# Performance work log

Hardware: AMD Instinct MI355X
Metric: run time of the kernel (lower is better)

Reference implementation:

```python
import jax, jax.numpy as jnp
import numpy as np

E, D, H, K, DIL, T = 8, 768, 3072, 3, 1, 16384


def _conv1d(x, w, b, dilation):
    # x: [1, C_in, L]; w: [C_out, C_in, K]; torch Conv1d with SAME padding
    pad = dilation * (w.shape[-1] - 1) // 2
    y = jax.lax.conv_general_dilated(
        x, w, window_strides=(1,), padding=[(pad, pad)],
        rhs_dilation=(dilation,), dimension_numbers=("NCH", "OIH", "NCH"))
    return y + b[None, :, None]


def setup_inputs() -> dict:
    key = jax.random.key(0)
    k0, k1, k2, k3, k4 = jax.random.split(key, 5)
    inp = jax.random.normal(k0, (T, D), dtype=jnp.float32)
    fwd_expert_count = jnp.full((E,), T // E, dtype=jnp.int32)
    w1 = jax.random.normal(k1, (E, H, D, K), dtype=jnp.float32) * (1.0 / np.sqrt(D * K))
    b1 = jax.random.normal(k2, (E, H), dtype=jnp.float32) * 0.01
    w2 = jax.random.normal(k3, (E, D, H, K), dtype=jnp.float32) * (1.0 / np.sqrt(H * K))
    b2 = jax.random.normal(k4, (E, D), dtype=jnp.float32) * 0.01
    return {"inp": inp, "fwd_expert_count": fwd_expert_count,
            "w1": w1, "b1": b1, "w2": w2, "b2": b2}


def reference(inp, fwd_expert_count, w1, b1, w2, b2):
    # counts define static per-expert segment lengths (constants w.r.t. compute graph)
    counts = np.asarray(jax.device_get(fwd_expert_count))
    x = inp.T[None]  # [1, D, T]
    outs, idx = [], 0
    for i in range(counts.shape[0]):
        n = int(counts[i])
        if n > 0:
            outs.append(_conv1d(x[:, :, idx:idx + n], w1[i], b1[i], DIL))
            idx += n
    h = jax.nn.gelu(jnp.concatenate(outs, axis=2), approximate=False)  # [1, H, T]
    outs, idx = [], 0
    for i in range(counts.shape[0]):
        n = int(counts[i])
        if n > 0:
            outs.append(_conv1d(h[:, :, idx:idx + n], w2[i], b2[i], DIL))
            idx += n
    y = jnp.concatenate(outs, axis=2)[0]  # [D, T]
    return y.T  # [T, D]
```

## Files before the change

kernel.cpp:

```cpp
#include <hip/hip_runtime.h>
#include <hip/hip_bf16.h>
#include <cstdint>

#define E_   8
#define D_   768
#define H_   3072
#define T_   16384
#define SEG  2048
#define PSEG (SEG + 2)

typedef __attribute__((ext_vector_type(8))) __bf16 bf16x8;
typedef __attribute__((ext_vector_type(4))) float f32x4;
typedef __attribute__((ext_vector_type(4))) unsigned int u32x4;

__device__ inline unsigned short f2bf(float f) {
  union { float f; unsigned int u; } v; v.f = f;
  unsigned int u = v.u;
  u += 0x7fffu + ((u >> 16) & 1u);
  return (unsigned short)(u >> 16);
}

__device__ inline float gelu_fast(float x) {
  const float a = -2.302118131f;
  const float b = -0.102944213f;
  float z = x * __builtin_fmaf(b, x * x, a);
  float e = __builtin_amdgcn_exp2f(z);
  return x * __builtin_amdgcn_rcpf(1.0f + e);
}

__device__ inline void gload16(const unsigned short* g, unsigned short* l) {
  __builtin_amdgcn_global_load_lds(
      (const __attribute__((address_space(1))) unsigned int*)g,
      (__attribute__((address_space(3))) unsigned int*)l, 16, 0, 0);
}

__global__ __launch_bounds__(256) void cvt_x_pad_kernel(const float* __restrict__ in,
                                                        unsigned short* __restrict__ out) {
  const int i = blockIdx.x * 256 + threadIdx.x;
  const int elem = i * 8;
  const int row = elem / D_;
  const int col = elem - row * D_;
  const int prow = (row >> 11) * PSEG + 1 + (row & (SEG - 1));
  const float* p = in + (size_t)row * D_ + col;
  u32x4 v;
#pragma unroll
  for (int j = 0; j < 4; ++j)
    v[j] = (unsigned)f2bf(p[2 * j]) | ((unsigned)f2bf(p[2 * j + 1]) << 16);
  *(u32x4*)(out + (size_t)prow * D_ + col) = v;
}

__global__ __launch_bounds__(256) void zero_guards_kernel(unsigned short* __restrict__ buf,
                                                          int C) {
  const int e = blockIdx.x >> 1;
  const size_t row = (size_t)e * PSEG + (blockIdx.x & 1) * (PSEG - 1);
  for (int c = threadIdx.x; c < C; c += 256) buf[row * C + c] = 0;
}

__global__ __launch_bounds__(256) void cvt_w_kernel(const float* __restrict__ in,
                                                    unsigned short* __restrict__ out,
                                                    int C) {
  int r = blockIdx.x;
  const float* src = in + (size_t)r * C * 3;
  unsigned short* dst = out + (size_t)r * C * 3;
  for (int c = threadIdx.x; c < C; c += 256) {
    float v0 = src[c * 3 + 0], v1 = src[c * 3 + 1], v2 = src[c * 3 + 2];
    dst[0 * C + c] = f2bf(v0);
    dst[1 * C + c] = f2bf(v1);
    dst[2 * C + c] = f2bf(v2);
  }
}

template <int CIN, int COUT, bool DO_GELU>
__global__ __launch_bounds__(512, 2) void conv_gemm8_kernel(
    const unsigned short* __restrict__ A,
    const unsigned short* __restrict__ Bt,
    const float* __restrict__ bias,
    void* __restrict__ Out) {
  __shared__ __align__(16) unsigned short lds[65536];

  constexpr int CSTEPS = CIN / 64;
  constexpr int NT = 3 * CSTEPS;
  constexpr int NTN = COUT / 256;

  const int tid  = threadIdx.x;
  const int wid  = tid >> 6, lane = tid & 63;
  const int wm   = wid >> 2, wn = wid & 3;

  const int bid = blockIdx.x;
  const int e   = bid & 7;
  const int rem = bid >> 3;
  const int mc  = rem / (4 * NTN);
  const int r2  = rem - mc * 4 * NTN;
  const int m0  = (mc * 4 + (r2 & 3)) * 256;
  const int n0  = (r2 >> 2) * 256;

  const int rowoff = tid >> 3;
  const int psrc   = ((lane & 7) ^ (lane >> 3)) * 8;
  const int ko     = (lane >> 4) * 16;
  const int ax     = (lane & 7) << 4;

  const size_t abase = ((size_t)e * PSEG + m0) * CIN;

  f32x4 acc[8][4];
#pragma unroll
  for (int n = 0; n < 4; ++n) {
    const float bv = bias[e * COUT + n0 + wn * 64 + n * 16 + (lane & 15)];
#pragma unroll
    for (int m = 0; m < 8; ++m) acc[m][n] = (f32x4){bv, bv, bv, bv};
  }

#define STAGE_A(kt_, part_) do {                                                     \
    const int ktu_ = (kt_);                                                          \
    const int ktc_ = ktu_ < NT ? ktu_ : NT - 1;    \
    const int k3_  = ktc_ / CSTEPS;                                                  \
    const int c0_  = (ktc_ - k3_ * CSTEPS) * 64;                                     \
    const int buf_ = ktu_ & 1;                                                       \
    _Pragma("unroll")                                                                \
    for (int ii_ = 0; ii_ < 2; ++ii_) {                                              \
      gload16(A + abase + (size_t)(ii_ * 128 + (part_) * 64 + rowoff + k3_) * CIN    \
                  + c0_ + psrc,                                                      \
              (unsigned short*)((char*)lds + buf_ * 32768 + ii_ * 16384 +            \
                                (part_) * 8192 + wid * 1024 + lane * 16));           \
    }                                                                                \
  } while (0)

#define STAGE_B(kt_, h_) do {                                                        \
    const int ktu_ = (kt_);                                                          \
    const int ktc_ = ktu_ < NT ? ktu_ : NT - 1;                                      \
    const int k3_  = ktc_ / CSTEPS;                                                  \
    const int c0_  = (ktc_ - k3_ * CSTEPS) * 64;                                     \
    const int buf_ = ktu_ & 1;                                                       \
    _Pragma("unroll")                                                                \
    for (int ii_ = 0; ii_ < 2; ++ii_) {                                              \
      const int brow_ = n0 + (h_) * 128 + ii_ * 64 + rowoff;                         \
      gload16(Bt + ((size_t)(e * COUT + brow_) * 3 + k3_) * CIN + c0_ + psrc,        \
              (unsigned short*)((char*)lds + 65536 + buf_ * 32768 + (h_) * 16384 +  \
                                ii_ * 8192 + wid * 1024 + lane * 16));               \
    }                                                                                \
  } while (0)

#define FULLBAR() do { asm volatile("" ::: "memory");                                \
                       __builtin_amdgcn_s_barrier();                                 \
                       asm volatile("" ::: "memory"); } while (0)
#define VM6() asm volatile("s_waitcnt vmcnt(6)" ::: "memory")
#define VM4() asm volatile("s_waitcnt vmcnt(4)" ::: "memory")
#define VM_NONE()

#define RA(buf_, mq_, s_, raA_, raB_, RB_) do {                                      \
    const char* Ab_ = (const char*)lds + (buf_) * 32768 + wm * 16384;                \
    if (RB_) {                                                                       \
      const char* Bb_ = (const char*)lds + 65536 + (buf_) * 32768 + (wn >> 1) * 16384; \
      _Pragma("unroll")                                                              \
      for (int n_ = 0; n_ < 4; ++n_)                                                 \
        raB_[n_] = *(const bf16x8*)(Bb_ +                                            \
            ((wn & 1) * 64 + n_ * 16 + (lane & 15)) * 128 + (((s_) * 64 + ko) ^ ax)); \
    }                                                                                \
    _Pragma("unroll")                                                                \
    for (int mi_ = 0; mi_ < 4; ++mi_)                                                \
      raA_[mi_] = *(const bf16x8*)(Ab_ +                                             \
          (((mq_) * 4 + mi_) * 16 + (lane & 15)) * 128 + (((s_) * 64 + ko) ^ ax));   \
  } while (0)

#define PHASE(raBuf_, raMq_, raS_, raA_, raB_, RB_, useA_, useB_, mq_, STAGE_STMT, VMW_) \
  do {                                                                               \
    FULLBAR();                                                                       \
    RA(raBuf_, raMq_, raS_, raA_, raB_, RB_);                                        \
    STAGE_STMT;                                                                      \
    __builtin_amdgcn_s_setprio(1);                                                   \
    _Pragma("unroll")                                                                \
    for (int mi_ = 0; mi_ < 4; ++mi_)                                                \
      _Pragma("unroll")                                                              \
      for (int n_ = 0; n_ < 4; ++n_)                                                 \
        acc[(mq_) * 4 + mi_][n_] = __builtin_amdgcn_mfma_f32_16x16x32_bf16(          \
            useA_[mi_], useB_[n_], acc[(mq_) * 4 + mi_][n_], 0, 0, 0);               \
    __builtin_amdgcn_s_setprio(0);                                                   \
    VMW_();                                                                          \
  } while (0)

  STAGE_B(0, 0); STAGE_B(0, 1); STAGE_A(0, 0); STAGE_A(0, 1);
  STAGE_B(1, 0); STAGE_B(1, 1);
  VM6();
  FULLBAR();

  bf16x8 aFA[4], aFB[4], bFA[4], bFB[4];
  RA(0, 0, 0, aFA, bFA, 1);

  int kt0 = 0;
#pragma unroll 1
  for (int it = 0; it < NT / 2; ++it, kt0 += 2) {
    PHASE(0,    0,   1,   aFB, bFB, 1, aFA, bFA, 0, STAGE_A(kt0 + 1, 0), VM6);
    PHASE(0,    1,   0,   aFA, bFA, 0, aFB, bFB, 0, STAGE_A(kt0 + 1, 1), VM_NONE);
    PHASE(0,    1,   1,   aFB, bFB, 0, aFA, bFA, 1, STAGE_B(kt0 + 2, 0), VM4);
    PHASE(1,    0,   0,   aFA, bFA, 1, aFB, bFB, 1, STAGE_B(kt0 + 2, 1), VM_NONE);
    PHASE(1,    0,   1,   aFB, bFB, 1, aFA, bFA, 0, STAGE_A(kt0 + 2, 0), VM6);
    PHASE(1,    1,   0,   aFA, bFA, 0, aFB, bFB, 0, STAGE_A(kt0 + 2, 1), VM_NONE);
    PHASE(1,    1,   1,   aFB, bFB, 0, aFA, bFA, 1, STAGE_B(kt0 + 3, 0), VM4);
    PHASE(0,    0,   0,   aFA, bFA, 1, aFB, bFB, 1, STAGE_B(kt0 + 3, 1), VM_NONE);
  }

  asm volatile("s_waitcnt vmcnt(0)" ::: "memory");

#undef PHASE
#undef RA
#undef STAGE_A
#undef STAGE_B
#undef FULLBAR
#undef VM6
#undef VM4
#undef VM_NONE

#pragma unroll
  for (int m = 0; m < 8; ++m) {
    const int rowb = m0 + wm * 128 + m * 16 + ((lane >> 4) << 2);
#pragma unroll
    for (int n = 0; n < 4; ++n) {
      const int col = n0 + wn * 64 + n * 16 + (lane & 15);
#pragma unroll
      for (int i = 0; i < 4; ++i) {
        if (DO_GELU) {
          const size_t off = ((size_t)e * PSEG + 1 + rowb + i) * COUT + col;
          ((unsigned short*)Out)[off] = f2bf(gelu_fast(acc[m][n][i]));
        } else {
          const size_t off = ((size_t)e * SEG + rowb + i) * COUT + col;
          ((float*)Out)[off] = acc[m][n][i];
        }
      }
    }
  }
}

extern "C" void kernel_launch(void* const* d_in, const int* in_sizes, int n_in,
                              void* d_out, int out_size, void* d_ws, size_t ws_size,
                              hipStream_t stream) {
  const float* inp = (const float*)d_in[0];
  const float* w1 = (const float*)d_in[2];
  const float* b1 = (const float*)d_in[3];
  const float* w2 = (const float*)d_in[4];
  const float* b2 = (const float*)d_in[5];
  float* out = (float*)d_out;
  char* ws = (char*)d_ws;

  const size_t szXp = (size_t)E_ * PSEG * D_ * 2;
  const size_t szHp = (size_t)E_ * PSEG * H_ * 2;
  const size_t szW1 = (size_t)E_ * H_ * 3 * D_ * 2;
  const size_t szW2 = (size_t)E_ * D_ * 3 * H_ * 2;

  unsigned short* Xp  = (unsigned short*)ws;
  unsigned short* Hp  = (unsigned short*)(ws + szXp);
  unsigned short* W1T = (unsigned short*)(ws + szXp + szHp);
  unsigned short* W2T = (unsigned short*)(ws + szXp + szHp + szW1);

  if (ws_size < szXp + szHp + szW1 + szW2) return;

  zero_guards_kernel<<<E_ * 2, 256, 0, stream>>>(Xp, D_);
  zero_guards_kernel<<<E_ * 2, 256, 0, stream>>>(Hp, H_);
  cvt_x_pad_kernel<<<T_ * D_ / 8 / 256, 256, 0, stream>>>(inp, Xp);
  cvt_w_kernel<<<E_ * H_, 256, 0, stream>>>(w1, W1T, D_);
  cvt_w_kernel<<<E_ * D_, 256, 0, stream>>>(w2, W2T, H_);

  constexpr int NWG1 = (H_ / 256) * (SEG / 256) * E_;
  constexpr int NWG2 = (D_ / 256) * (SEG / 256) * E_;
  conv_gemm8_kernel<D_, H_, true>
      <<<NWG1, 512, 0, stream>>>(Xp, W1T, b1, Hp);
  conv_gemm8_kernel<H_, D_, false>
      <<<NWG2, 512, 0, stream>>>(Hp, W2T, b2, out);
}
```

Baseline: 552.4 us.

## Switch GEMM inner loop to 32x32x16 MFMA with incremental load pointers

```diff
diff --git a/kernel.cpp b/kernel.cpp
--- a/kernel.cpp
+++ b/kernel.cpp
@@ -10,7 +10,7 @@
 #define PSEG (SEG + 2)
 
 typedef __attribute__((ext_vector_type(8))) __bf16 bf16x8;
-typedef __attribute__((ext_vector_type(4))) float f32x4;
+typedef __attribute__((ext_vector_type(16))) float f32x16;
 typedef __attribute__((ext_vector_type(4))) unsigned int u32x4;
 
 __device__ inline unsigned short f2bf(float f) {
@@ -96,47 +96,45 @@
 
   const int rowoff = tid >> 3;
   const int psrc   = ((lane & 7) ^ (lane >> 3)) * 8;
-  const int ko     = (lane >> 4) * 16;
   const int ax     = (lane & 7) << 4;
-
-  const size_t abase = ((size_t)e * PSEG + m0) * CIN;
-
-  f32x4 acc[8][4];
-#pragma unroll
-  for (int n = 0; n < 4; ++n) {
-    const float bv = bias[e * COUT + n0 + wn * 64 + n * 16 + (lane & 15)];
-#pragma unroll
-    for (int m = 0; m < 8; ++m) acc[m][n] = (f32x4){bv, bv, bv, bv};
-  }
-
-#define STAGE_A(kt_, part_) do {                                                     \
-    const int ktu_ = (kt_);                                                          \
-    const int ktc_ = ktu_ < NT ? ktu_ : NT - 1;    \
-    const int k3_  = ktc_ / CSTEPS;                                                  \
-    const int c0_  = (ktc_ - k3_ * CSTEPS) * 64;                                     \
-    const int buf_ = ktu_ & 1;                                                       \
-    _Pragma("unroll")                                                                \
-    for (int ii_ = 0; ii_ < 2; ++ii_) {                                              \
-      gload16(A + abase + (size_t)(ii_ * 128 + (part_) * 64 + rowoff + k3_) * CIN    \
-                  + c0_ + psrc,                                                      \
-              (unsigned short*)((char*)lds + buf_ * 32768 + ii_ * 16384 +            \
+  const int l31    = lane & 31;
+  const int kg     = (lane >> 5) * 16;
+
+  const unsigned short* aPtr = A + ((size_t)e * PSEG + m0 + rowoff) * CIN + psrc;
+  const unsigned short* bPtr = Bt + ((size_t)(e * COUT + n0 + rowoff)) * 3 * CIN + psrc;
+
+  f32x16 acc[4][2];
+#pragma unroll
+  for (int nf = 0; nf < 2; ++nf) {
+    const float bv = bias[e * COUT + n0 + wn * 64 + nf * 32 + l31];
+    f32x16 z;
+#pragma unroll
+    for (int r = 0; r < 16; ++r) z[r] = bv;
+#pragma unroll
+    for (int mf = 0; mf < 4; ++mf) acc[mf][nf] = z;
+  }
+
+#define ADV(ptr_, j_) do {                                                           \
+    const int nx_ = (j_) + 1;                                                        \
+    const int d_  = (nx_ >= NT) ? 0                                                  \
+                  : ((nx_ % CSTEPS) == 0 ? (CIN - (CSTEPS - 1) * 64) : 64);          \
+    ptr_ += d_;                                                                      \
+  } while (0)
+
+#define STAGE_A(BUF_, part_) do {                                                    \
+    _Pragma("unroll")                                                                \
+    for (int ii_ = 0; ii_ < 2; ++ii_)                                                \
+      gload16(aPtr + (size_t)(ii_ * 128 + (part_) * 64) * CIN,                       \
+              (unsigned short*)((char*)lds + (BUF_) * 32768 + ii_ * 16384 +          \
                                 (part_) * 8192 + wid * 1024 + lane * 16));           \
-    }                                                                                \
-  } while (0)
-
-#define STAGE_B(kt_, h_) do {                                                        \
-    const int ktu_ = (kt_);                                                          \
-    const int ktc_ = ktu_ < NT ? ktu_ : NT - 1;                                      \
-    const int k3_  = ktc_ / CSTEPS;                                                  \
-    const int c0_  = (ktc_ - k3_ * CSTEPS) * 64;                                     \
-    const int buf_ = ktu_ & 1;                                                       \
-    _Pragma("unroll")                                                                \
-    for (int ii_ = 0; ii_ < 2; ++ii_) {                                              \
-      const int brow_ = n0 + (h_) * 128 + ii_ * 64 + rowoff;                         \
-      gload16(Bt + ((size_t)(e * COUT + brow_) * 3 + k3_) * CIN + c0_ + psrc,        \
-              (unsigned short*)((char*)lds + 65536 + buf_ * 32768 + (h_) * 16384 +  \
+  } while (0)
+
+#define STAGE_B(BUF_, h_) do {                                                       \
+    _Pragma("unroll")                                                                \
+    for (int ii_ = 0; ii_ < 2; ++ii_)                                                \
+      gload16(bPtr + (size_t)((h_) * 128 + ii_ * 64) * 3 * CIN,                      \
+              (unsigned short*)((char*)lds + 65536 + (BUF_) * 32768 + (h_) * 16384 + \
                                 ii_ * 8192 + wid * 1024 + lane * 16));               \
-    }                                                                                \
   } while (0)
 
 #define FULLBAR() do { asm volatile("" ::: "memory");                                \
@@ -146,83 +144,93 @@
 #define VM4() asm volatile("s_waitcnt vmcnt(4)" ::: "memory")
 #define VM_NONE()
 
-#define RA(buf_, mq_, s_, raA_, raB_, RB_) do {                                      \
-    const char* Ab_ = (const char*)lds + (buf_) * 32768 + wm * 16384;                \
-    if (RB_) {                                                                       \
-      const char* Bb_ = (const char*)lds + 65536 + (buf_) * 32768 + (wn >> 1) * 16384; \
+#define RA_A(buf_, mh_, ksp_, dst_) do {                                             \
+    const char* Ab_ = (const char*)lds + (buf_) * 32768 +                            \
+                      (wm * 128 + (mh_) * 64 + l31) * 128;                           \
+    _Pragma("unroll")                                                                \
+    for (int mf_ = 0; mf_ < 2; ++mf_)                                                \
       _Pragma("unroll")                                                              \
-      for (int n_ = 0; n_ < 4; ++n_)                                                 \
-        raB_[n_] = *(const bf16x8*)(Bb_ +                                            \
-            ((wn & 1) * 64 + n_ * 16 + (lane & 15)) * 128 + (((s_) * 64 + ko) ^ ax)); \
-    }                                                                                \
-    _Pragma("unroll")                                                                \
-    for (int mi_ = 0; mi_ < 4; ++mi_)                                                \
-      raA_[mi_] = *(const bf16x8*)(Ab_ +                                             \
-          (((mq_) * 4 + mi_) * 16 + (lane & 15)) * 128 + (((s_) * 64 + ko) ^ ax));   \
-  } while (0)
-
-#define PHASE(raBuf_, raMq_, raS_, raA_, raB_, RB_, useA_, useB_, mq_, STAGE_STMT, VMW_) \
-  do {                                                                               \
-    FULLBAR();                                                                       \
-    RA(raBuf_, raMq_, raS_, raA_, raB_, RB_);                                        \
-    STAGE_STMT;                                                                      \
+      for (int ki_ = 0; ki_ < 2; ++ki_)                                              \
+        dst_[mf_ * 2 + ki_] = *(const bf16x8*)(Ab_ + mf_ * 4096 +                    \
+            ((((ksp_) * 2 + ki_) * 32 + kg) ^ ax));                                  \
+  } while (0)
+
+#define RA_B(buf_, ksp_, dst_) do {                                                  \
+    const char* Bb_ = (const char*)lds + 65536 + (buf_) * 32768 +                    \
+                      (wn * 64 + l31) * 128;                                         \
+    _Pragma("unroll")                                                                \
+    for (int nf_ = 0; nf_ < 2; ++nf_)                                                \
+      _Pragma("unroll")                                                              \
+      for (int ki_ = 0; ki_ < 2; ++ki_)                                              \
+        dst_[nf_ * 2 + ki_] = *(const bf16x8*)(Bb_ + nf_ * 4096 +                    \
+            ((((ksp_) * 2 + ki_) * 32 + kg) ^ ax));                                  \
+  } while (0)
+
+#define MFMA8(mh_, aU_, bU_) do {                                                    \
     __builtin_amdgcn_s_setprio(1);                                                   \
     _Pragma("unroll")                                                                \
-    for (int mi_ = 0; mi_ < 4; ++mi_)                                                \
+    for (int ki_ = 0; ki_ < 2; ++ki_)                                                \
       _Pragma("unroll")                                                              \
-      for (int n_ = 0; n_ < 4; ++n_)                                                 \
-        acc[(mq_) * 4 + mi_][n_] = __builtin_amdgcn_mfma_f32_16x16x32_bf16(          \
-            useA_[mi_], useB_[n_], acc[(mq_) * 4 + mi_][n_], 0, 0, 0);               \
+      for (int mf_ = 0; mf_ < 2; ++mf_)                                              \
+        _Pragma("unroll")                                                            \
+        for (int nf_ = 0; nf_ < 2; ++nf_)                                            \
+          acc[(mh_) * 2 + mf_][nf_] = __builtin_amdgcn_mfma_f32_32x32x16_bf16(       \
+              aU_[mf_ * 2 + ki_], bU_[nf_ * 2 + ki_], acc[(mh_) * 2 + mf_][nf_],     \
+              0, 0, 0);                                                              \
     __builtin_amdgcn_s_setprio(0);                                                   \
-    VMW_();                                                                          \
-  } while (0)
-
-  STAGE_B(0, 0); STAGE_B(0, 1); STAGE_A(0, 0); STAGE_A(0, 1);
-  STAGE_B(1, 0); STAGE_B(1, 1);
+  } while (0)
+
+  STAGE_B(0, 0); STAGE_B(0, 1); ADV(bPtr, 0);
+  STAGE_A(0, 0); STAGE_A(0, 1); ADV(aPtr, 0);
+  STAGE_B(1, 0); STAGE_B(1, 1); ADV(bPtr, 1);
   VM6();
   FULLBAR();
 
-  bf16x8 aFA[4], aFB[4], bFA[4], bFB[4];
-  RA(0, 0, 0, aFA, bFA, 1);
+  bf16x8 aX[4], aY[4], bF0[4], bF1[4];
+  RA_A(0, 0, 0, aX);
+  RA_B(0, 0, bF0);
 
   int kt0 = 0;
 #pragma unroll 1
   for (int it = 0; it < NT / 2; ++it, kt0 += 2) {
-    PHASE(0,    0,   1,   aFB, bFB, 1, aFA, bFA, 0, STAGE_A(kt0 + 1, 0), VM6);
-    PHASE(0,    1,   0,   aFA, bFA, 0, aFB, bFB, 0, STAGE_A(kt0 + 1, 1), VM_NONE);
-    PHASE(0,    1,   1,   aFB, bFB, 0, aFA, bFA, 1, STAGE_B(kt0 + 2, 0), VM4);
-    PHASE(1,    0,   0,   aFA, bFA, 1, aFB, bFB, 1, STAGE_B(kt0 + 2, 1), VM_NONE);
-    PHASE(1,    0,   1,   aFB, bFB, 1, aFA, bFA, 0, STAGE_A(kt0 + 2, 0), VM6);
-    PHASE(1,    1,   0,   aFA, bFA, 0, aFB, bFB, 0, STAGE_A(kt0 + 2, 1), VM_NONE);
-    PHASE(1,    1,   1,   aFB, bFB, 0, aFA, bFA, 1, STAGE_B(kt0 + 3, 0), VM4);
-    PHASE(0,    0,   0,   aFA, bFA, 1, aFB, bFB, 1, STAGE_B(kt0 + 3, 1), VM_NONE);
+    FULLBAR(); RA_A(0, 0, 1, aY); RA_B(0, 1, bF1); STAGE_A(1, 0); MFMA8(0, aX, bF0); VM6();
+    FULLBAR(); RA_A(0, 1, 0, aX);                  STAGE_A(1, 1); MFMA8(0, aY, bF1); ADV(aPtr, kt0 + 1);
+    FULLBAR(); RA_A(0, 1, 1, aY);                  STAGE_B(0, 0); MFMA8(1, aX, bF0); VM4();
+    FULLBAR(); RA_A(1, 0, 0, aX); RA_B(1, 0, bF0); STAGE_B(0, 1); MFMA8(1, aY, bF1); ADV(bPtr, kt0 + 2);
+    FULLBAR(); RA_A(1, 0, 1, aY); RA_B(1, 1, bF1); STAGE_A(0, 0); MFMA8(0, aX, bF0); VM6();
+    FULLBAR(); RA_A(1, 1, 0, aX);                  STAGE_A(0, 1); MFMA8(0, aY, bF1); ADV(aPtr, kt0 + 2);
+    FULLBAR(); RA_A(1, 1, 1, aY);                  STAGE_B(1, 0); MFMA8(1, aX, bF0); VM4();
+    FULLBAR(); RA_A(0, 0, 0, aX); RA_B(0, 0, bF0); STAGE_B(1, 1); MFMA8(1, aY, bF1); ADV(bPtr, kt0 + 3);
   }
 
   asm volatile("s_waitcnt vmcnt(0)" ::: "memory");
 
-#undef PHASE
-#undef RA
+#undef MFMA8
+#undef RA_A
+#undef RA_B
 #undef STAGE_A
 #undef STAGE_B
+#undef ADV
 #undef FULLBAR
 #undef VM6
 #undef VM4
 #undef VM_NONE
 
 #pragma unroll
-  for (int m = 0; m < 8; ++m) {
-    const int rowb = m0 + wm * 128 + m * 16 + ((lane >> 4) << 2);
-#pragma unroll
-    for (int n = 0; n < 4; ++n) {
-      const int col = n0 + wn * 64 + n * 16 + (lane & 15);
-#pragma unroll
-      for (int i = 0; i < 4; ++i) {
+  for (int mf = 0; mf < 4; ++mf) {
+    const int rowb = m0 + wm * 128 + mf * 32 + 4 * (lane >> 5);
+#pragma unroll
+    for (int nf = 0; nf < 2; ++nf) {
+      const int col = n0 + wn * 64 + nf * 32 + l31;
+#pragma unroll
+      for (int r = 0; r < 16; ++r) {
+        const int row = rowb + (r & 3) + 8 * (r >> 2);
         if (DO_GELU) {
-          const size_t off = ((size_t)e * PSEG + 1 + rowb + i) * COUT + col;
-          ((unsigned short*)Out)[off] = f2bf(gelu_fast(acc[m][n][i]));
+          const size_t off = ((size_t)e * PSEG + 1 + row) * COUT + col;
+          ((unsigned short*)Out)[off] = f2bf(gelu_fast(acc[mf][nf][r]));
         } else {
-          const size_t off = ((size_t)e * SEG + rowb + i) * COUT + col;
-          ((float*)Out)[off] = acc[m][n][i];
+          const size_t off = ((size_t)e * SEG + row) * COUT + col;
+          ((float*)Out)[off] = acc[mf][nf][r];
         }
       }
     }
```

Measured after the change: 588.8 us. 6.6% more time.

## Add 256x192-tile conv GEMM kernel for second layer to fill all CUs

Applied to the files above, without the earlier changes.

```diff
diff --git a/kernel.cpp b/kernel.cpp
--- a/kernel.cpp
+++ b/kernel.cpp
@@ -111,7 +111,7 @@
 
 #define STAGE_A(kt_, part_) do {                                                     \
     const int ktu_ = (kt_);                                                          \
-    const int ktc_ = ktu_ < NT ? ktu_ : NT - 1;    \
+    const int ktc_ = ktu_ < NT ? ktu_ : NT - 1;                                      \
     const int k3_  = ktc_ / CSTEPS;                                                  \
     const int c0_  = (ktc_ - k3_ * CSTEPS) * 64;                                     \
     const int buf_ = ktu_ & 1;                                                       \
@@ -119,7 +119,7 @@
     for (int ii_ = 0; ii_ < 2; ++ii_) {                                              \
       gload16(A + abase + (size_t)(ii_ * 128 + (part_) * 64 + rowoff + k3_) * CIN    \
                   + c0_ + psrc,                                                      \
-              (unsigned short*)((char*)lds + buf_ * 32768 + ii_ * 16384 +            \
+              (unsigned short*)((char*)lds + (buf_) * 32768 + ii_ * 16384 +          \
                                 (part_) * 8192 + wid * 1024 + lane * 16));           \
     }                                                                                \
   } while (0)
@@ -134,7 +134,7 @@
     for (int ii_ = 0; ii_ < 2; ++ii_) {                                              \
       const int brow_ = n0 + (h_) * 128 + ii_ * 64 + rowoff;                         \
       gload16(Bt + ((size_t)(e * COUT + brow_) * 3 + k3_) * CIN + c0_ + psrc,        \
-              (unsigned short*)((char*)lds + 65536 + buf_ * 32768 + (h_) * 16384 +  \
+              (unsigned short*)((char*)lds + 65536 + (buf_) * 32768 + (h_) * 16384 + \
                                 ii_ * 8192 + wid * 1024 + lane * 16));               \
     }                                                                                \
   } while (0)
@@ -188,14 +188,14 @@
   int kt0 = 0;
 #pragma unroll 1
   for (int it = 0; it < NT / 2; ++it, kt0 += 2) {
-    PHASE(0,    0,   1,   aFB, bFB, 1, aFA, bFA, 0, STAGE_A(kt0 + 1, 0), VM6);
-    PHASE(0,    1,   0,   aFA, bFA, 0, aFB, bFB, 0, STAGE_A(kt0 + 1, 1), VM_NONE);
-    PHASE(0,    1,   1,   aFB, bFB, 0, aFA, bFA, 1, STAGE_B(kt0 + 2, 0), VM4);
-    PHASE(1,    0,   0,   aFA, bFA, 1, aFB, bFB, 1, STAGE_B(kt0 + 2, 1), VM_NONE);
-    PHASE(1,    0,   1,   aFB, bFB, 1, aFA, bFA, 0, STAGE_A(kt0 + 2, 0), VM6);
-    PHASE(1,    1,   0,   aFA, bFA, 0, aFB, bFB, 0, STAGE_A(kt0 + 2, 1), VM_NONE);
-    PHASE(1,    1,   1,   aFB, bFB, 0, aFA, bFA, 1, STAGE_B(kt0 + 3, 0), VM4);
-    PHASE(0,    0,   0,   aFA, bFA, 1, aFB, bFB, 1, STAGE_B(kt0 + 3, 1), VM_NONE);
+    PHASE(0, 0, 1, aFB, bFB, 1, aFA, bFA, 0, STAGE_A(kt0 + 1, 0), VM6);
+    PHASE(0, 1, 0, aFA, bFA, 0, aFB, bFB, 0, STAGE_A(kt0 + 1, 1), VM_NONE);
+    PHASE(0, 1, 1, aFB, bFB, 0, aFA, bFA, 1, STAGE_B(kt0 + 2, 0), VM4);
+    PHASE(1, 0, 0, aFA, bFA, 1, aFB, bFB, 1, STAGE_B(kt0 + 2, 1), VM_NONE);
+    PHASE(1, 0, 1, aFB, bFB, 1, aFA, bFA, 0, STAGE_A(kt0 + 2, 0), VM6);
+    PHASE(1, 1, 0, aFA, bFA, 0, aFB, bFB, 0, STAGE_A(kt0 + 2, 1), VM_NONE);
+    PHASE(1, 1, 1, aFB, bFB, 0, aFA, bFA, 1, STAGE_B(kt0 + 3, 0), VM4);
+    PHASE(0, 0, 0, aFA, bFA, 1, aFB, bFB, 1, STAGE_B(kt0 + 3, 1), VM_NONE);
   }
 
   asm volatile("s_waitcnt vmcnt(0)" ::: "memory");
@@ -204,10 +204,6 @@
 #undef RA
 #undef STAGE_A
 #undef STAGE_B
-#undef FULLBAR
-#undef VM6
-#undef VM4
-#undef VM_NONE
 
 #pragma unroll
   for (int m = 0; m < 8; ++m) {
@@ -227,6 +223,155 @@
       }
     }
   }
+#undef FULLBAR
+#undef VM6
+#undef VM4
+#undef VM_NONE
+}
+
+template <int CIN, int COUT>
+__global__ __launch_bounds__(512, 2) void conv_gemm_n192_kernel(
+    const unsigned short* __restrict__ A,
+    const unsigned short* __restrict__ Bt,
+    const float* __restrict__ bias,
+    float* __restrict__ Out) {
+  __shared__ __align__(16) unsigned short lds[57344];
+
+  constexpr int CSTEPS = CIN / 64;
+  constexpr int NT = 3 * CSTEPS;
+
+  const int tid  = threadIdx.x;
+  const int wid  = tid >> 6, lane = tid & 63;
+  const int wm   = wid >> 2, wn = wid & 3;
+
+  const int bid = blockIdx.x;
+  const int e   = bid & 7;
+  const int rem = bid >> 3;
+  const int m0  = (rem & 7) * 256;
+  const int n0  = (rem >> 3) * 192;
+
+  const int rowoff = tid >> 3;
+  const int psrc   = ((lane & 7) ^ (lane >> 3)) * 8;
+  const int ko     = (lane >> 4) * 16;
+  const int ax     = (lane & 7) << 4;
+  const int l15    = lane & 15;
+
+  const unsigned short* aPtr = A + ((size_t)e * PSEG + m0 + rowoff) * CIN + psrc;
+  const unsigned short* bPtr = Bt + (size_t)(e * COUT + n0 + rowoff) * 3 * CIN + psrc;
+
+  f32x4 acc[8][3];
+#pragma unroll
+  for (int n = 0; n < 3; ++n) {
+    const float bv = bias[e * COUT + n0 + wn * 48 + n * 16 + l15];
+#pragma unroll
+    for (int m = 0; m < 8; ++m) acc[m][n] = (f32x4){bv, bv, bv, bv};
+  }
+
+#define ADV(ptr_, j_) do {                                                           \
+    const int nx_ = (j_) + 1;                                                        \
+    const int d_  = (nx_ >= NT) ? 0                                                  \
+                  : ((nx_ % CSTEPS) == 0 ? (CIN - (CSTEPS - 1) * 64) : 64);          \
+    ptr_ += d_;                                                                      \
+  } while (0)
+
+#define STAGE_A2(BUF_, slot_)                                                        \
+  gload16(aPtr + (size_t)((slot_) * 64) * CIN,                                       \
+          (unsigned short*)((char*)lds + (BUF_) * 32768 + (slot_) * 8192 +           \
+                            wid * 1024 + lane * 16))
+#define STAGE_B2(BUF_, slot_)                                                        \
+  gload16(bPtr + (size_t)((slot_) * 64) * 3 * CIN,                                   \
+          (unsigned short*)((char*)lds + 65536 + (BUF_) * 24576 + (slot_) * 8192 +   \
+                            wid * 1024 + lane * 16))
+
+#define FULLBAR() do { asm volatile("" ::: "memory");                                \
+                       __builtin_amdgcn_s_barrier();                                 \
+                       asm volatile("" ::: "memory"); } while (0)
+#define VM3() asm volatile("s_waitcnt vmcnt(3)" ::: "memory")
+#define VM2() asm volatile("s_waitcnt vmcnt(2)" ::: "memory")
+
+#define RA_A2(buf_, mq_, s_, dst_) do {                                              \
+    const char* Ab_ = (const char*)lds + (buf_) * 32768;                             \
+    _Pragma("unroll")                                                                \
+    for (int mi_ = 0; mi_ < 4; ++mi_)                                                \
+      dst_[mi_] = *(const bf16x8*)(Ab_ +                                             \
+          (wm * 128 + ((mq_) * 4 + mi_) * 16 + l15) * 128 + (((s_) * 64 + ko) ^ ax)); \
+  } while (0)
+
+#define RA_B2(buf_, s_, dst_) do {                                                   \
+    const char* Bb_ = (const char*)lds + 65536 + (buf_) * 24576;                     \
+    _Pragma("unroll")                                                                \
+    for (int n_ = 0; n_ < 3; ++n_)                                                   \
+      dst_[n_] = *(const bf16x8*)(Bb_ +                                              \
+          (wn * 48 + n_ * 16 + l15) * 128 + (((s_) * 64 + ko) ^ ax));                \
+  } while (0)
+
+#define MFMA12(mq_, aU_, bU_) do {                                                   \
+    __builtin_amdgcn_s_setprio(1);                                                   \
+    _Pragma("unroll")                                                                \
+    for (int mi_ = 0; mi_ < 4; ++mi_)                                                \
+      _Pragma("unroll")                                                              \
+      for (int n_ = 0; n_ < 3; ++n_)                                                 \
+        acc[(mq_) * 4 + mi_][n_] = __builtin_amdgcn_mfma_f32_16x16x32_bf16(          \
+            aU_[mi_], bU_[n_], acc[(mq_) * 4 + mi_][n_], 0, 0, 0);                   \
+    __builtin_amdgcn_s_setprio(0);                                                   \
+  } while (0)
+
+  STAGE_A2(0, 0); STAGE_A2(0, 1); STAGE_A2(0, 2); STAGE_A2(0, 3); ADV(aPtr, 0);
+  STAGE_B2(0, 0); STAGE_B2(0, 1); STAGE_B2(0, 2); ADV(bPtr, 0);
+  STAGE_B2(1, 0); STAGE_B2(1, 1); STAGE_B2(1, 2); ADV(bPtr, 1);
+  VM3();
+  FULLBAR();
+
+  bf16x8 aX[4], aY[4], bF0[3], bF1[3];
+  RA_A2(0, 0, 0, aX);
+  RA_B2(0, 0, bF0);
+
+  int kt0 = 0;
+#pragma unroll 1
+  for (int it = 0; it < NT / 2; ++it, kt0 += 2) {
+    FULLBAR(); RA_A2(0, 0, 1, aY); RA_B2(0, 1, bF1);
+               STAGE_A2(1, 0); STAGE_A2(1, 1); STAGE_A2(1, 2); STAGE_A2(1, 3);
+               ADV(aPtr, kt0 + 1); MFMA12(0, aX, bF0);
+    FULLBAR(); RA_A2(0, 1, 0, aX); MFMA12(0, aY, bF1);
+    FULLBAR(); RA_A2(0, 1, 1, aY); STAGE_B2(0, 0); STAGE_B2(0, 1);
+               MFMA12(1, aX, bF0); VM2();
+    FULLBAR(); RA_A2(1, 0, 0, aX); RA_B2(1, 0, bF0); STAGE_B2(0, 2);
+               ADV(bPtr, kt0 + 2); MFMA12(1, aY, bF1);
+    FULLBAR(); RA_A2(1, 0, 1, aY); RA_B2(1, 1, bF1);
+               STAGE_A2(0, 0); STAGE_A2(0, 1); STAGE_A2(0, 2); STAGE_A2(0, 3);
+               ADV(aPtr, kt0 + 2); MFMA12(0, aX, bF0);
+    FULLBAR(); RA_A2(1, 1, 0, aX); MFMA12(0, aY, bF1);
+    FULLBAR(); RA_A2(1, 1, 1, aY); STAGE_B2(1, 0); STAGE_B2(1, 1);
+               MFMA12(1, aX, bF0); VM2();
+    FULLBAR(); RA_A2(0, 0, 0, aX); RA_B2(0, 0, bF0); STAGE_B2(1, 2);
+               ADV(bPtr, kt0 + 3); MFMA12(1, aY, bF1);
+  }
+
+  asm volatile("s_waitcnt vmcnt(0)" ::: "memory");
+
+#undef MFMA12
+#undef RA_A2
+#undef RA_B2
+#undef STAGE_A2
+#undef STAGE_B2
+#undef ADV
+#undef FULLBAR
+#undef VM3
+#undef VM2
+
+#pragma unroll
+  for (int m = 0; m < 8; ++m) {
+    const int rowb = m0 + wm * 128 + m * 16 + ((lane >> 4) << 2);
+#pragma unroll
+    for (int n = 0; n < 3; ++n) {
+      const int col = n0 + wn * 48 + n * 16 + l15;
+#pragma unroll
+      for (int i = 0; i < 4; ++i) {
+        const size_t off = ((size_t)e * SEG + rowb + i) * COUT + col;
+        Out[off] = acc[m][n][i];
+      }
+    }
+  }
 }
 
 extern "C" void kernel_launch(void* const* d_in, const int* in_sizes, int n_in,
@@ -259,9 +404,9 @@
   cvt_w_kernel<<<E_ * D_, 256, 0, stream>>>(w2, W2T, H_);
 
   constexpr int NWG1 = (H_ / 256) * (SEG / 256) * E_;
-  constexpr int NWG2 = (D_ / 256) * (SEG / 256) * E_;
+  constexpr int NWG2 = (D_ / 192) * (SEG / 256) * E_;
   conv_gemm8_kernel<D_, H_, true>
       <<<NWG1, 512, 0, stream>>>(Xp, W1T, b1, Hp);
-  conv_gemm8_kernel<H_, D_, false>
+  conv_gemm_n192_kernel<H_, D_>
       <<<NWG2, 512, 0, stream>>>(Hp, W2T, b2, out);
 }
```

After: 530.6 us. -3.9%, faster.
